# Performance work log

Hardware: AMD Instinct MI355X
Metric: run time of the kernel (lower is better)

## Reference

```python
import jax, jax.numpy as jnp
import numpy as np

EPS = 1e-7  # K.epsilon()
ROUTINGS = 3


def squash(v, axis=-1):
    s2 = jnp.sum(jnp.square(v), axis=axis, keepdims=True)
    scale = s2 / (1.0 + s2) / jnp.sqrt(s2 + EPS)
    return scale * v


def setup_inputs() -> dict:
    key = jax.random.key(0)
    k1, k2 = jax.random.split(key)
    B, I, D_IN = 64, 2048, 16
    J, D_OUT = 32, 32
    inputs = jax.random.normal(k1, (B, I, D_IN), dtype=jnp.float32)
    W = jax.random.normal(k2, (J, I, D_OUT, D_IN), dtype=jnp.float32) * 0.05
    return {"inputs": inputs, "W": W}


def reference(inputs, W):
    # u_hat[b,j,i,e] = sum_d inputs[b,i,d] * W[j,i,e,d]
    u_hat = jnp.einsum('bid,jied->bjie', inputs, W)  # [B, J, I, D_out]
    B, J, I, _ = u_hat.shape
    b = jnp.zeros((B, J, I), dtype=u_hat.dtype)
    outputs = None
    for r in range(ROUTINGS):
        c = jax.nn.softmax(b, axis=1)                 # softmax over output capsules J
        s = jnp.einsum('bji,bjie->bje', c, u_hat)     # weighted sum over input capsules
        outputs = squash(s)                           # [B, J, D_out]
        if r < ROUTINGS - 1:
            b = b + jnp.einsum('bje,bjie->bji', outputs, u_hat)
    return outputs
```

## Files before the change

### kernel.cpp

```cpp
#include <hip/hip_runtime.h>
#include <hip/hip_bf16.h>

#define NB 64
#define NI 2048
#define ND 16
#define NJ 32
#define NE 32
#define NIP (NI/2)
#define NKC 32
#define NSL NKC

typedef __attribute__((ext_vector_type(8))) short bfrag;
typedef __attribute__((ext_vector_type(4))) float f32x4;

__device__ inline unsigned pk2bf(float a, float b) {
    __hip_bfloat162 h = __float22bfloat162_rn(make_float2(a, b));
    return *reinterpret_cast<unsigned*>(&h);
}

template <int N>
__device__ inline float rot16_add(float v) {
    int r = __builtin_amdgcn_mov_dpp(__float_as_int(v), 0x120 + N, 0xf, 0xf, false);
    return v + __int_as_float(r);
}

__device__ inline unsigned scale_pair(unsigned u, float cc) {
    float f0 = __uint_as_float(u << 16);
    float f1 = __uint_as_float(u & 0xffff0000u);
    return pk2bf(f0 * cc, f1 * cc);
}

__global__ __launch_bounds__(256) void convxT_k(const float* __restrict__ x,
                                                short* __restrict__ xT)
{
    const int T = blockIdx.x * 256 + threadIdx.x;
    const int i = T >> 6, b = T & 63;
    const float4* src = reinterpret_cast<const float4*>(
        x + ((size_t)b * NI + i) * ND);
    float4 a0 = src[0], a1 = src[1], a2 = src[2], a3 = src[3];
    bfrag lo, hi;
    unsigned* lu = reinterpret_cast<unsigned*>(&lo);
    unsigned* hu = reinterpret_cast<unsigned*>(&hi);
    lu[0] = pk2bf(a0.x, a0.y); lu[1] = pk2bf(a0.z, a0.w);
    lu[2] = pk2bf(a1.x, a1.y); lu[3] = pk2bf(a1.z, a1.w);
    hu[0] = pk2bf(a2.x, a2.y); hu[1] = pk2bf(a2.z, a2.w);
    hu[2] = pk2bf(a3.x, a3.y); hu[3] = pk2bf(a3.z, a3.w);
    short* dst = xT + ((size_t)i * NB + b) * ND;
    *reinterpret_cast<bfrag*>(dst)     = lo;
    *reinterpret_cast<bfrag*>(dst + 8) = hi;
}

__global__ __launch_bounds__(512) void lgsm_k(
    const short* __restrict__ xT,
    const short* __restrict__ Wb,
    const float* __restrict__ Oacc,
    float* __restrict__ c)
{
    const int l    = blockIdx.x;
    const int grp  = l >> 5;
    const int bb   = (l >> 3) & 3;
    const int ic   = grp * 8 + (l & 7);
    const int b0   = bb * 16;
    const int i0   = ic * 16;
    const int t    = threadIdx.x;
    const int wv   = t >> 6;
    const int ln   = t & 63;
    const int m    = ln & 15;
    const int quad = ln >> 4;

    __shared__ float lp[NJ][16][16];

    float O0[4][4], O1[4][4];
#pragma unroll
    for (int jj = 0; jj < 4; ++jj) {
        const int j = wv * 4 + jj;
#pragma unroll
        for (int r = 0; r < 4; ++r) {
            const int b = b0 + quad * 4 + r;
            O0[jj][r] = Oacc[((size_t)b * NJ + j) * NE + m];
            O1[jj][r] = Oacc[((size_t)b * NJ + j) * NE + 16 + m];
        }
    }

    const int  bA  = b0 + m;
    const bool act = quad < 2;
    const int  d0  = quad * 8;

    for (int il = 0; il < 16; ++il) {
        const int i = i0 + il;
        const int ip = i >> 1, isel = i & 1;
        bfrag av = (bfrag)0;
        if (act) {
            av = *reinterpret_cast<const bfrag*>(
                xT + ((size_t)i * NB + bA) * ND + d0);
        }
#pragma unroll
        for (int jj = 0; jj < 4; ++jj) {
            const int j = wv * 4 + jj;
            bfrag bv0 = (bfrag)0, bv1 = (bfrag)0;
            if (act) {
                const short* wp = Wb + (((size_t)j * NIP + ip) * NE + m) * 32
                                     + isel * 16 + d0;
                bv0 = *reinterpret_cast<const bfrag*>(wp);
                bv1 = *reinterpret_cast<const bfrag*>(wp + 16 * 32);
            }
            f32x4 z = {0.f, 0.f, 0.f, 0.f};
            f32x4 U0 = __builtin_amdgcn_mfma_f32_16x16x32_bf16(av, bv0, z, 0, 0, 0);
            f32x4 U1 = __builtin_amdgcn_mfma_f32_16x16x32_bf16(av, bv1, z, 0, 0, 0);

            float v4[4];
#pragma unroll
            for (int r = 0; r < 4; ++r) {
                float v = fmaf(U0[r], O0[jj][r], U1[r] * O1[jj][r]);
                v = rot16_add<1>(v);
                v = rot16_add<2>(v);
                v = rot16_add<4>(v);
                v = rot16_add<8>(v);
                v4[r] = v;
            }
            if (m == 0) {
                *reinterpret_cast<float4*>(&lp[j][il][quad * 4]) =
                    make_float4(v4[0], v4[1], v4[2], v4[3]);
            }
        }
    }
    __syncthreads();

    if (t < 256) {
        const int i = t >> 4, b = t & 15;
        float v[NJ];
        float mx = -1e30f;
#pragma unroll
        for (int jx = 0; jx < NJ; ++jx) {
            v[jx] = lp[jx][i][b];
            mx = fmaxf(mx, v[jx]);
        }
        float sum = 0.f;
#pragma unroll
        for (int jx = 0; jx < NJ; ++jx) {
            v[jx] = __expf(v[jx] - mx);
            sum += v[jx];
        }
        const float inv = 1.0f / sum;
#pragma unroll
        for (int jx = 0; jx < NJ; ++jx)
            c[((size_t)jx * NI + i0 + i) * NB + b0 + b] = v[jx] * inv;
    }
}

template <bool R0>
__global__ __launch_bounds__(256, 4) void wsum_k(
    const float* __restrict__ Wsrc,
    const short* __restrict__ xT,
    short* __restrict__ Wb,
    const float* __restrict__ c,
    float* __restrict__ partial)
{
    const int j    = blockIdx.x;
    const int kc   = blockIdx.y;
    const int t    = threadIdx.x;
    const int wv   = t >> 6;
    const int ln   = t & 63;
    const int m    = ln & 15;
    const int quad = ln >> 4;
    const int isel = quad >> 1;
    const int d0   = (quad & 1) * 8;
    const int ip0  = kc * 32 + wv * 8;

    __shared__ float red[4][2048];

    f32x4 acc[4][2];
#pragma unroll
    for (int a = 0; a < 4; ++a)
#pragma unroll
        for (int n = 0; n < 2; ++n) acc[a][n] = (f32x4){0.f, 0.f, 0.f, 0.f};

#pragma unroll 2
    for (int it = 0; it < 8; ++it) {
        const int ip = ip0 + it;
        const int ia = ip * 2 + isel;
        bfrag bv0, bv1;
        if (R0) {
            const float* wp0 = Wsrc + (((size_t)j * NI + ia) * NE + m) * ND + d0;
            float4 w0 = *reinterpret_cast<const float4*>(wp0);
            float4 w1 = *reinterpret_cast<const float4*>(wp0 + 4);
            float4 w2 = *reinterpret_cast<const float4*>(wp0 + 16 * ND);
            float4 w3 = *reinterpret_cast<const float4*>(wp0 + 16 * ND + 4);
            unsigned* b0u = reinterpret_cast<unsigned*>(&bv0);
            unsigned* b1u = reinterpret_cast<unsigned*>(&bv1);
            b0u[0] = pk2bf(w0.x, w0.y); b0u[1] = pk2bf(w0.z, w0.w);
            b0u[2] = pk2bf(w1.x, w1.y); b0u[3] = pk2bf(w1.z, w1.w);
            b1u[0] = pk2bf(w2.x, w2.y); b1u[1] = pk2bf(w2.z, w2.w);
            b1u[2] = pk2bf(w3.x, w3.y); b1u[3] = pk2bf(w3.z, w3.w);
            short* wd = Wb + (((size_t)j * NIP + ip) * NE + m) * 32 + quad * 8;
            *reinterpret_cast<bfrag*>(wd)       = bv0;
            *reinterpret_cast<bfrag*>(wd + 512) = bv1;
        } else {
            const short* wp = Wb + (((size_t)j * NIP + ip) * NE + m) * 32 + quad * 8;
            bv0 = *reinterpret_cast<const bfrag*>(wp);
            bv1 = *reinterpret_cast<const bfrag*>(wp + 512);
        }
#pragma unroll
        for (int mt = 0; mt < 4; ++mt) {
            const int b = mt * 16 + m;
            const float cc = R0 ? (1.0f / NJ)
                                : c[((size_t)j * NI + ia) * NB + b];
            const uint4 xr = *reinterpret_cast<const uint4*>(
                xT + ((size_t)ia * NB + b) * ND + d0);
            bfrag av;
            unsigned* avu = reinterpret_cast<unsigned*>(&av);
            avu[0] = scale_pair(xr.x, cc);
            avu[1] = scale_pair(xr.y, cc);
            avu[2] = scale_pair(xr.z, cc);
            avu[3] = scale_pair(xr.w, cc);
            acc[mt][0] = __builtin_amdgcn_mfma_f32_16x16x32_bf16(av, bv0, acc[mt][0], 0, 0, 0);
            acc[mt][1] = __builtin_amdgcn_mfma_f32_16x16x32_bf16(av, bv1, acc[mt][1], 0, 0, 0);
        }
    }

    float* rb = &red[wv][0];
#pragma unroll
    for (int mt = 0; mt < 4; ++mt)
#pragma unroll
        for (int nt = 0; nt < 2; ++nt)
            *reinterpret_cast<f32x4*>(rb + (mt * 2 + nt) * 256 + ln * 4)
                = acc[mt][nt];
    __syncthreads();

    float* pb = partial + ((size_t)kc * NJ + j) * 2048;
    {
        const int g = t * 4;
        f32x4 s0 = *reinterpret_cast<const f32x4*>(&red[0][g]);
        s0 += *reinterpret_cast<const f32x4*>(&red[1][g]);
        s0 += *reinterpret_cast<const f32x4*>(&red[2][g]);
        s0 += *reinterpret_cast<const f32x4*>(&red[3][g]);
        f32x4 s1 = *reinterpret_cast<const f32x4*>(&red[0][1024 + g]);
        s1 += *reinterpret_cast<const f32x4*>(&red[1][1024 + g]);
        s1 += *reinterpret_cast<const f32x4*>(&red[2][1024 + g]);
        s1 += *reinterpret_cast<const f32x4*>(&red[3][1024 + g]);
        *reinterpret_cast<f32x4*>(pb + g)        = s0;
        *reinterpret_cast<f32x4*>(pb + 1024 + g) = s1;
    }
}

__global__ __launch_bounds__(512) void rs_k(
    const float* __restrict__ partial,
    float* __restrict__ Oacc,
    float* __restrict__ out,
    int mode)
{
    const int G    = blockIdx.x * 512 + threadIdx.x;
    const int j    = G >> 11;
    const int g    = G & 2047;
    const int group = g >> 8;
    const int mt   = group >> 1;
    const int nt   = group & 1;
    const int lnn  = (g >> 2) & 63;
    const int m    = lnn & 15;
    const int quad = lnn >> 4;
    const int r    = g & 3;
    const int b    = mt * 16 + quad * 4 + r;
    const int e    = nt * 16 + m;

    float sum = 0.f;
#pragma unroll 8
    for (int sl = 0; sl < NSL; ++sl)
        sum += partial[((size_t)sl * NJ + j) * 2048 + g];

    __shared__ float lds[512];
    const int row = quad * 4 + r;
    lds[row * 32 + e] = sum;
    __syncthreads();
    const float* rp = &lds[row * 32];
    float p = 0.f;
#pragma unroll
    for (int ee = 0; ee < 32; ++ee) p = fmaf(rp[ee], rp[ee], p);

    const float scale = p / ((1.0f + p) * sqrtf(p + 1e-7f));
    const float o = scale * sum;
    const size_t off = ((size_t)b * NJ + j) * NE + e;
    if (mode == 2)      out[off]  = o;
    else if (mode == 1) Oacc[off] += o;
    else                Oacc[off] = o;
}

extern "C" void kernel_launch(void* const* d_in, const int* in_sizes, int n_in,
                              void* d_out, int out_size, void* d_ws, size_t ws_size,
                              hipStream_t stream)
{
    (void)in_sizes; (void)n_in; (void)out_size; (void)ws_size;
    const float* x = (const float*)d_in[0];
    const float* W = (const float*)d_in[1];
    float* out = (float*)d_out;

    float* Oacc = (float*)d_ws;
    float* c    = Oacc + NB * NJ * NE;
    float* part = c + (size_t)NJ * NI * NB;
    short* Wb   = (short*)(part + (size_t)NSL * NJ * 2048);
    short* xT   = Wb + (size_t)NJ * NIP * NE * 32;

    convxT_k<<<(NI * NB) / 256, 256, 0, stream>>>(x, xT);

    dim3 gW(NJ, NKC);

    wsum_k<true><<<gW, 256, 0, stream>>>(W, xT, Wb, c, part);
    rs_k<<<65536 / 512, 512, 0, stream>>>(part, Oacc, out, 0);

    lgsm_k<<<512, 512, 0, stream>>>(xT, Wb, Oacc, c);
    wsum_k<false><<<gW, 256, 0, stream>>>(W, xT, Wb, c, part);
    rs_k<<<65536 / 512, 512, 0, stream>>>(part, Oacc, out, 1);

    lgsm_k<<<512, 512, 0, stream>>>(xT, Wb, Oacc, c);
    wsum_k<false><<<gW, 256, 0, stream>>>(W, xT, Wb, c, part);
    rs_k<<<65536 / 512, 512, 0, stream>>>(part, Oacc, out, 2);
}
```

Measured before the change: 391.1 us.

## Double-buffer wsum loads and split work across more, smaller blocks

```diff
diff --git a/kernel.cpp b/kernel.cpp
--- a/kernel.cpp
+++ b/kernel.cpp
@@ -7,7 +7,7 @@
 #define NJ 32
 #define NE 32
 #define NIP (NI/2)
-#define NKC 32
+#define NKC 64
 #define NSL NKC
 
 typedef __attribute__((ext_vector_type(8))) short bfrag;
@@ -149,7 +149,7 @@
 }
 
 template <bool R0>
-__global__ __launch_bounds__(256, 4) void wsum_k(
+__global__ __launch_bounds__(128, 4) void wsum_k(
     const float* __restrict__ Wsrc,
     const short* __restrict__ xT,
     short* __restrict__ Wb,
@@ -165,9 +165,9 @@
     const int quad = ln >> 4;
     const int isel = quad >> 1;
     const int d0   = (quad & 1) * 8;
-    const int ip0  = kc * 32 + wv * 8;
-
-    __shared__ float red[4][2048];
+    const int ip0  = kc * 16 + wv * 8;
+
+    __shared__ float red[2][2048];
 
     f32x4 acc[4][2];
 #pragma unroll
@@ -175,47 +175,76 @@
 #pragma unroll
         for (int n = 0; n < 2; ++n) acc[a][n] = (f32x4){0.f, 0.f, 0.f, 0.f};
 
-#pragma unroll 2
-    for (int it = 0; it < 8; ++it) {
+    struct Stage {
+        bfrag  bv0, bv1;
+        float4 w0, w1, w2, w3;
+        uint4  xr[4];
+        float  cc[4];
+    };
+
+    auto load = [&](Stage& S, int it) {
         const int ip = ip0 + it;
         const int ia = ip * 2 + isel;
+        if constexpr (R0) {
+            const float* wp0 = Wsrc + (((size_t)j * NI + ia) * NE + m) * ND + d0;
+            S.w0 = *reinterpret_cast<const float4*>(wp0);
+            S.w1 = *reinterpret_cast<const float4*>(wp0 + 4);
+            S.w2 = *reinterpret_cast<const float4*>(wp0 + 16 * ND);
+            S.w3 = *reinterpret_cast<const float4*>(wp0 + 16 * ND + 4);
+        } else {
+            const short* wp = Wb + (((size_t)j * NIP + ip) * NE + m) * 32 + quad * 8;
+            S.bv0 = *reinterpret_cast<const bfrag*>(wp);
+            S.bv1 = *reinterpret_cast<const bfrag*>(wp + 512);
+        }
+#pragma unroll
+        for (int mt = 0; mt < 4; ++mt) {
+            const int b = mt * 16 + m;
+            if constexpr (!R0)
+                S.cc[mt] = c[((size_t)j * NI + ia) * NB + b];
+            S.xr[mt] = *reinterpret_cast<const uint4*>(
+                xT + ((size_t)ia * NB + b) * ND + d0);
+        }
+    };
+
+    auto compute = [&](Stage& S, int it) {
         bfrag bv0, bv1;
-        if (R0) {
-            const float* wp0 = Wsrc + (((size_t)j * NI + ia) * NE + m) * ND + d0;
-            float4 w0 = *reinterpret_cast<const float4*>(wp0);
-            float4 w1 = *reinterpret_cast<const float4*>(wp0 + 4);
-            float4 w2 = *reinterpret_cast<const float4*>(wp0 + 16 * ND);
-            float4 w3 = *reinterpret_cast<const float4*>(wp0 + 16 * ND + 4);
+        if constexpr (R0) {
             unsigned* b0u = reinterpret_cast<unsigned*>(&bv0);
             unsigned* b1u = reinterpret_cast<unsigned*>(&bv1);
-            b0u[0] = pk2bf(w0.x, w0.y); b0u[1] = pk2bf(w0.z, w0.w);
-            b0u[2] = pk2bf(w1.x, w1.y); b0u[3] = pk2bf(w1.z, w1.w);
-            b1u[0] = pk2bf(w2.x, w2.y); b1u[1] = pk2bf(w2.z, w2.w);
-            b1u[2] = pk2bf(w3.x, w3.y); b1u[3] = pk2bf(w3.z, w3.w);
+            b0u[0] = pk2bf(S.w0.x, S.w0.y); b0u[1] = pk2bf(S.w0.z, S.w0.w);
+            b0u[2] = pk2bf(S.w1.x, S.w1.y); b0u[3] = pk2bf(S.w1.z, S.w1.w);
+            b1u[0] = pk2bf(S.w2.x, S.w2.y); b1u[1] = pk2bf(S.w2.z, S.w2.w);
+            b1u[2] = pk2bf(S.w3.x, S.w3.y); b1u[3] = pk2bf(S.w3.z, S.w3.w);
+            const int ip = ip0 + it;
             short* wd = Wb + (((size_t)j * NIP + ip) * NE + m) * 32 + quad * 8;
             *reinterpret_cast<bfrag*>(wd)       = bv0;
             *reinterpret_cast<bfrag*>(wd + 512) = bv1;
         } else {
-            const short* wp = Wb + (((size_t)j * NIP + ip) * NE + m) * 32 + quad * 8;
-            bv0 = *reinterpret_cast<const bfrag*>(wp);
-            bv1 = *reinterpret_cast<const bfrag*>(wp + 512);
+            bv0 = S.bv0; bv1 = S.bv1;
         }
 #pragma unroll
         for (int mt = 0; mt < 4; ++mt) {
-            const int b = mt * 16 + m;
-            const float cc = R0 ? (1.0f / NJ)
-                                : c[((size_t)j * NI + ia) * NB + b];
-            const uint4 xr = *reinterpret_cast<const uint4*>(
-                xT + ((size_t)ia * NB + b) * ND + d0);
+            const float cc = R0 ? (1.0f / NJ) : S.cc[mt];
             bfrag av;
             unsigned* avu = reinterpret_cast<unsigned*>(&av);
-            avu[0] = scale_pair(xr.x, cc);
-            avu[1] = scale_pair(xr.y, cc);
-            avu[2] = scale_pair(xr.z, cc);
-            avu[3] = scale_pair(xr.w, cc);
+            avu[0] = scale_pair(S.xr[mt].x, cc);
+            avu[1] = scale_pair(S.xr[mt].y, cc);
+            avu[2] = scale_pair(S.xr[mt].z, cc);
+            avu[3] = scale_pair(S.xr[mt].w, cc);
             acc[mt][0] = __builtin_amdgcn_mfma_f32_16x16x32_bf16(av, bv0, acc[mt][0], 0, 0, 0);
             acc[mt][1] = __builtin_amdgcn_mfma_f32_16x16x32_bf16(av, bv1, acc[mt][1], 0, 0, 0);
         }
+    };
+
+    Stage sA, sB;
+    load(sA, 0);
+    load(sB, 1);
+#pragma unroll
+    for (int it = 0; it < 8; it += 2) {
+        compute(sA, it);
+        if (it + 2 < 8) load(sA, it + 2);
+        compute(sB, it + 1);
+        if (it + 3 < 8) load(sB, it + 3);
     }
 
     float* rb = &red[wv][0];
@@ -228,18 +257,12 @@
     __syncthreads();
 
     float* pb = partial + ((size_t)kc * NJ + j) * 2048;
-    {
-        const int g = t * 4;
-        f32x4 s0 = *reinterpret_cast<const f32x4*>(&red[0][g]);
-        s0 += *reinterpret_cast<const f32x4*>(&red[1][g]);
-        s0 += *reinterpret_cast<const f32x4*>(&red[2][g]);
-        s0 += *reinterpret_cast<const f32x4*>(&red[3][g]);
-        f32x4 s1 = *reinterpret_cast<const f32x4*>(&red[0][1024 + g]);
-        s1 += *reinterpret_cast<const f32x4*>(&red[1][1024 + g]);
-        s1 += *reinterpret_cast<const f32x4*>(&red[2][1024 + g]);
-        s1 += *reinterpret_cast<const f32x4*>(&red[3][1024 + g]);
-        *reinterpret_cast<f32x4*>(pb + g)        = s0;
-        *reinterpret_cast<f32x4*>(pb + 1024 + g) = s1;
+#pragma unroll
+    for (int k = 0; k < 4; ++k) {
+        const int g = k * 512 + t * 4;
+        f32x4 s = *reinterpret_cast<const f32x4*>(&red[0][g]);
+        s += *reinterpret_cast<const f32x4*>(&red[1][g]);
+        *reinterpret_cast<f32x4*>(pb + g) = s;
     }
 }
 
@@ -303,14 +326,14 @@
 
     dim3 gW(NJ, NKC);
 
-    wsum_k<true><<<gW, 256, 0, stream>>>(W, xT, Wb, c, part);
+    wsum_k<true><<<gW, 128, 0, stream>>>(W, xT, Wb, c, part);
     rs_k<<<65536 / 512, 512, 0, stream>>>(part, Oacc, out, 0);
 
     lgsm_k<<<512, 512, 0, stream>>>(xT, Wb, Oacc, c);
-    wsum_k<false><<<gW, 256, 0, stream>>>(W, xT, Wb, c, part);
+    wsum_k<false><<<gW, 128, 0, stream>>>(W, xT, Wb, c, part);
     rs_k<<<65536 / 512, 512, 0, stream>>>(part, Oacc, out, 1);
 
     lgsm_k<<<512, 512, 0, stream>>>(xT, Wb, Oacc, c);
-    wsum_k<false><<<gW, 256, 0, stream>>>(W, xT, Wb, c, part);
+    wsum_k<false><<<gW, 128, 0, stream>>>(W, xT, Wb, c, part);
     rs_k<<<65536 / 512, 512, 0, stream>>>(part, Oacc, out, 2);
 }
```

Result: faster. 381.9 us (-2.3%).

## Software-pipeline wsum loads, halve block size, double split-K with XCD-aware block swizzle

Applied to the files above, without the earlier changes.

```diff
diff --git a/kernel.cpp b/kernel.cpp
--- a/kernel.cpp
+++ b/kernel.cpp
@@ -7,7 +7,7 @@
 #define NJ 32
 #define NE 32
 #define NIP (NI/2)
-#define NKC 32
+#define NKC 64
 #define NSL NKC
 
 typedef __attribute__((ext_vector_type(8))) short bfrag;
@@ -148,16 +148,73 @@
     }
 }
 
+
+#define WS_LOAD(P, itv)                                                        \
+    {   const int ip_ = ip0 + (itv);                                           \
+        const int ia_ = ip_ * 2 + isel;                                        \
+        if constexpr (R0) {                                                    \
+            const float* wp_ = Wsrc + (((size_t)j * NI + ia_) * NE + m) * ND + d0; \
+            P##w0 = *reinterpret_cast<const float4*>(wp_);                     \
+            P##w1 = *reinterpret_cast<const float4*>(wp_ + 4);                 \
+            P##w2 = *reinterpret_cast<const float4*>(wp_ + 16 * ND);           \
+            P##w3 = *reinterpret_cast<const float4*>(wp_ + 16 * ND + 4);       \
+        } else {                                                               \
+            const short* bp_ = Wb + (((size_t)j * NIP + ip_) * NE + m) * 32 + quad * 8; \
+            P##bv0 = *reinterpret_cast<const bfrag*>(bp_);                     \
+            P##bv1 = *reinterpret_cast<const bfrag*>(bp_ + 512);               \
+            const float* cp_ = cbuf + ((size_t)j * NI + ia_) * NB + m;         \
+            P##c0 = cp_[0];  P##c1 = cp_[16];                                  \
+            P##c2 = cp_[32]; P##c3 = cp_[48];                                  \
+        }                                                                      \
+        const short* xp_ = xT + ((size_t)ia_ * NB + m) * ND + d0;              \
+        P##x0 = *reinterpret_cast<const uint4*>(xp_);                          \
+        P##x1 = *reinterpret_cast<const uint4*>(xp_ + 16 * ND);                \
+        P##x2 = *reinterpret_cast<const uint4*>(xp_ + 32 * ND);                \
+        P##x3 = *reinterpret_cast<const uint4*>(xp_ + 48 * ND);                \
+    }
+
+#define WS_MT(XV, CV, A0, A1)                                                  \
+    {   const float cc_ = R0 ? (1.0f / NJ) : (CV);                             \
+        bfrag av_;                                                             \
+        unsigned* au_ = reinterpret_cast<unsigned*>(&av_);                     \
+        au_[0] = scale_pair((XV).x, cc_); au_[1] = scale_pair((XV).y, cc_);    \
+        au_[2] = scale_pair((XV).z, cc_); au_[3] = scale_pair((XV).w, cc_);    \
+        A0 = __builtin_amdgcn_mfma_f32_16x16x32_bf16(av_, bv0_, A0, 0, 0, 0);  \
+        A1 = __builtin_amdgcn_mfma_f32_16x16x32_bf16(av_, bv1_, A1, 0, 0, 0);  \
+    }
+
+#define WS_COMPUTE(P, itv)                                                     \
+    {   bfrag bv0_, bv1_;                                                      \
+        if constexpr (R0) {                                                    \
+            unsigned* b0_ = reinterpret_cast<unsigned*>(&bv0_);                \
+            unsigned* b1_ = reinterpret_cast<unsigned*>(&bv1_);                \
+            b0_[0] = pk2bf(P##w0.x, P##w0.y); b0_[1] = pk2bf(P##w0.z, P##w0.w);\
+            b0_[2] = pk2bf(P##w1.x, P##w1.y); b0_[3] = pk2bf(P##w1.z, P##w1.w);\
+            b1_[0] = pk2bf(P##w2.x, P##w2.y); b1_[1] = pk2bf(P##w2.z, P##w2.w);\
+            b1_[2] = pk2bf(P##w3.x, P##w3.y); b1_[3] = pk2bf(P##w3.z, P##w3.w);\
+            short* wd_ = Wb + (((size_t)j * NIP + (ip0 + (itv))) * NE + m) * 32 + quad * 8; \
+            *reinterpret_cast<bfrag*>(wd_)       = bv0_;                       \
+            *reinterpret_cast<bfrag*>(wd_ + 512) = bv1_;                       \
+        } else { bv0_ = P##bv0; bv1_ = P##bv1; }                               \
+        WS_MT(P##x0, P##c0, a00, a01)                                          \
+        WS_MT(P##x1, P##c1, a10, a11)                                          \
+        WS_MT(P##x2, P##c2, a20, a21)                                          \
+        WS_MT(P##x3, P##c3, a30, a31)                                          \
+    }
+
 template <bool R0>
-__global__ __launch_bounds__(256, 4) void wsum_k(
+__global__ __launch_bounds__(128, 4) void wsum_k(
     const float* __restrict__ Wsrc,
     const short* __restrict__ xT,
     short* __restrict__ Wb,
-    const float* __restrict__ c,
+    const float* __restrict__ cbuf,
     float* __restrict__ partial)
 {
-    const int j    = blockIdx.x;
-    const int kc   = blockIdx.y;
+    const int l    = blockIdx.x;
+    const int x    = l & 7;
+    const int r    = l >> 3;
+    const int j    = r & 31;
+    const int kc   = x * 8 + (r >> 5);
     const int t    = threadIdx.x;
     const int wv   = t >> 6;
     const int ln   = t & 63;
@@ -165,81 +222,55 @@
     const int quad = ln >> 4;
     const int isel = quad >> 1;
     const int d0   = (quad & 1) * 8;
-    const int ip0  = kc * 32 + wv * 8;
-
-    __shared__ float red[4][2048];
-
-    f32x4 acc[4][2];
-#pragma unroll
-    for (int a = 0; a < 4; ++a)
-#pragma unroll
-        for (int n = 0; n < 2; ++n) acc[a][n] = (f32x4){0.f, 0.f, 0.f, 0.f};
-
-#pragma unroll 2
-    for (int it = 0; it < 8; ++it) {
-        const int ip = ip0 + it;
-        const int ia = ip * 2 + isel;
-        bfrag bv0, bv1;
-        if (R0) {
-            const float* wp0 = Wsrc + (((size_t)j * NI + ia) * NE + m) * ND + d0;
-            float4 w0 = *reinterpret_cast<const float4*>(wp0);
-            float4 w1 = *reinterpret_cast<const float4*>(wp0 + 4);
-            float4 w2 = *reinterpret_cast<const float4*>(wp0 + 16 * ND);
-            float4 w3 = *reinterpret_cast<const float4*>(wp0 + 16 * ND + 4);
-            unsigned* b0u = reinterpret_cast<unsigned*>(&bv0);
-            unsigned* b1u = reinterpret_cast<unsigned*>(&bv1);
-            b0u[0] = pk2bf(w0.x, w0.y); b0u[1] = pk2bf(w0.z, w0.w);
-            b0u[2] = pk2bf(w1.x, w1.y); b0u[3] = pk2bf(w1.z, w1.w);
-            b1u[0] = pk2bf(w2.x, w2.y); b1u[1] = pk2bf(w2.z, w2.w);
-            b1u[2] = pk2bf(w3.x, w3.y); b1u[3] = pk2bf(w3.z, w3.w);
-            short* wd = Wb + (((size_t)j * NIP + ip) * NE + m) * 32 + quad * 8;
-            *reinterpret_cast<bfrag*>(wd)       = bv0;
-            *reinterpret_cast<bfrag*>(wd + 512) = bv1;
-        } else {
-            const short* wp = Wb + (((size_t)j * NIP + ip) * NE + m) * 32 + quad * 8;
-            bv0 = *reinterpret_cast<const bfrag*>(wp);
-            bv1 = *reinterpret_cast<const bfrag*>(wp + 512);
-        }
-#pragma unroll
-        for (int mt = 0; mt < 4; ++mt) {
-            const int b = mt * 16 + m;
-            const float cc = R0 ? (1.0f / NJ)
-                                : c[((size_t)j * NI + ia) * NB + b];
-            const uint4 xr = *reinterpret_cast<const uint4*>(
-                xT + ((size_t)ia * NB + b) * ND + d0);
-            bfrag av;
-            unsigned* avu = reinterpret_cast<unsigned*>(&av);
-            avu[0] = scale_pair(xr.x, cc);
-            avu[1] = scale_pair(xr.y, cc);
-            avu[2] = scale_pair(xr.z, cc);
-            avu[3] = scale_pair(xr.w, cc);
-            acc[mt][0] = __builtin_amdgcn_mfma_f32_16x16x32_bf16(av, bv0, acc[mt][0], 0, 0, 0);
-            acc[mt][1] = __builtin_amdgcn_mfma_f32_16x16x32_bf16(av, bv1, acc[mt][1], 0, 0, 0);
-        }
-    }
+    const int ip0  = kc * 16 + wv * 8;
+
+    __shared__ float red[2][2048];
+
+    f32x4 a00 = {0.f,0.f,0.f,0.f}, a01 = {0.f,0.f,0.f,0.f};
+    f32x4 a10 = {0.f,0.f,0.f,0.f}, a11 = {0.f,0.f,0.f,0.f};
+    f32x4 a20 = {0.f,0.f,0.f,0.f}, a21 = {0.f,0.f,0.f,0.f};
+    f32x4 a30 = {0.f,0.f,0.f,0.f}, a31 = {0.f,0.f,0.f,0.f};
+
+    bfrag  Abv0, Abv1, Bbv0, Bbv1;
+    float4 Aw0, Aw1, Aw2, Aw3, Bw0, Bw1, Bw2, Bw3;
+    uint4  Ax0, Ax1, Ax2, Ax3, Bx0, Bx1, Bx2, Bx3;
+    float  Ac0, Ac1, Ac2, Ac3, Bc0, Bc1, Bc2, Bc3;
+
+    WS_LOAD(A, 0)
+    WS_LOAD(B, 1)
+    WS_COMPUTE(A, 0)
+    WS_LOAD(A, 2)
+    WS_COMPUTE(B, 1)
+    WS_LOAD(B, 3)
+    WS_COMPUTE(A, 2)
+    WS_LOAD(A, 4)
+    WS_COMPUTE(B, 3)
+    WS_LOAD(B, 5)
+    WS_COMPUTE(A, 4)
+    WS_LOAD(A, 6)
+    WS_COMPUTE(B, 5)
+    WS_LOAD(B, 7)
+    WS_COMPUTE(A, 6)
+    WS_COMPUTE(B, 7)
 
     float* rb = &red[wv][0];
-#pragma unroll
-    for (int mt = 0; mt < 4; ++mt)
-#pragma unroll
-        for (int nt = 0; nt < 2; ++nt)
-            *reinterpret_cast<f32x4*>(rb + (mt * 2 + nt) * 256 + ln * 4)
-                = acc[mt][nt];
+    *reinterpret_cast<f32x4*>(rb + 0 * 256 + ln * 4) = a00;
+    *reinterpret_cast<f32x4*>(rb + 1 * 256 + ln * 4) = a01;
+    *reinterpret_cast<f32x4*>(rb + 2 * 256 + ln * 4) = a10;
+    *reinterpret_cast<f32x4*>(rb + 3 * 256 + ln * 4) = a11;
+    *reinterpret_cast<f32x4*>(rb + 4 * 256 + ln * 4) = a20;
+    *reinterpret_cast<f32x4*>(rb + 5 * 256 + ln * 4) = a21;
+    *reinterpret_cast<f32x4*>(rb + 6 * 256 + ln * 4) = a30;
+    *reinterpret_cast<f32x4*>(rb + 7 * 256 + ln * 4) = a31;
     __syncthreads();
 
     float* pb = partial + ((size_t)kc * NJ + j) * 2048;
-    {
-        const int g = t * 4;
-        f32x4 s0 = *reinterpret_cast<const f32x4*>(&red[0][g]);
-        s0 += *reinterpret_cast<const f32x4*>(&red[1][g]);
-        s0 += *reinterpret_cast<const f32x4*>(&red[2][g]);
-        s0 += *reinterpret_cast<const f32x4*>(&red[3][g]);
-        f32x4 s1 = *reinterpret_cast<const f32x4*>(&red[0][1024 + g]);
-        s1 += *reinterpret_cast<const f32x4*>(&red[1][1024 + g]);
-        s1 += *reinterpret_cast<const f32x4*>(&red[2][1024 + g]);
-        s1 += *reinterpret_cast<const f32x4*>(&red[3][1024 + g]);
-        *reinterpret_cast<f32x4*>(pb + g)        = s0;
-        *reinterpret_cast<f32x4*>(pb + 1024 + g) = s1;
+#pragma unroll
+    for (int k = 0; k < 4; ++k) {
+        const int g = k * 512 + t * 4;
+        f32x4 s = *reinterpret_cast<const f32x4*>(&red[0][g]);
+        s += *reinterpret_cast<const f32x4*>(&red[1][g]);
+        *reinterpret_cast<f32x4*>(pb + g) = s;
     }
 }
 
@@ -301,16 +332,14 @@
 
     convxT_k<<<(NI * NB) / 256, 256, 0, stream>>>(x, xT);
 
-    dim3 gW(NJ, NKC);
-
-    wsum_k<true><<<gW, 256, 0, stream>>>(W, xT, Wb, c, part);
+    wsum_k<true><<<NJ * NKC, 128, 0, stream>>>(W, xT, Wb, c, part);
     rs_k<<<65536 / 512, 512, 0, stream>>>(part, Oacc, out, 0);
 
     lgsm_k<<<512, 512, 0, stream>>>(xT, Wb, Oacc, c);
-    wsum_k<false><<<gW, 256, 0, stream>>>(W, xT, Wb, c, part);
+    wsum_k<false><<<NJ * NKC, 128, 0, stream>>>(W, xT, Wb, c, part);
     rs_k<<<65536 / 512, 512, 0, stream>>>(part, Oacc, out, 1);
 
     lgsm_k<<<512, 512, 0, stream>>>(xT, Wb, Oacc, c);
-    wsum_k<false><<<gW, 256, 0, stream>>>(W, xT, Wb, c, part);
+    wsum_k<false><<<NJ * NKC, 128, 0, stream>>>(W, xT, Wb, c, part);
     rs_k<<<65536 / 512, 512, 0, stream>>>(part, Oacc, out, 2);
 }
```

Result: faster. 339.1 us (-13.3%).
